# Kernel tuning notes

Hardware: AMD Instinct MI355X
Metric: run time of the kernel (lower is better)

## Reference

```python
import jax, jax.numpy as jnp
import numpy as np
from jax.ops import segment_sum

N_NODES = 100000


def _deg_inv_sqrt(idx, n):
    # DGL GraphConv norm='both': degs clamped to min 1, then deg^{-0.5}
    deg = segment_sum(jnp.ones_like(idx, dtype=jnp.float32), idx, num_segments=n)
    return jnp.where(deg > 0, jax.lax.rsqrt(jnp.maximum(deg, 1.0)), 1.0)


def _graph_conv(x, src, dst, W, b, out_norm, in_norm, n):
    # norm='both': scale src feats by out_deg^-1/2, sum-aggregate, scale by in_deg^-1/2
    h = (x * out_norm[:, None]) @ W          # apply weight first (cheaper/equal width)
    msg = h[src]                              # [E, d] irregular gather
    agg = segment_sum(msg, dst, num_segments=n)
    return agg * in_norm[:, None] + b


def setup_inputs() -> dict:
    key = jax.random.key(0)
    k1, k2, k3, k4, k5, k6, k7 = jax.random.split(key, 7)
    E = 1600000
    in_feats, h_feats, out_feats = 128, 128, 64
    in_feat = jax.random.normal(k1, (N_NODES, in_feats), dtype=jnp.float32)
    src = jax.random.randint(k2, (E,), 0, N_NODES, dtype=jnp.int32)
    dst = jax.random.randint(k3, (E,), 0, N_NODES, dtype=jnp.int32)
    # Glorot-style init like dgl GraphConv
    W1 = jax.random.normal(k4, (in_feats, h_feats), dtype=jnp.float32) * (1.0 / np.sqrt(in_feats))
    b1 = jnp.zeros((h_feats,), dtype=jnp.float32)
    W2 = jax.random.normal(k5, (h_feats, out_feats), dtype=jnp.float32) * (1.0 / np.sqrt(h_feats))
    b2 = jnp.zeros((out_feats,), dtype=jnp.float32)
    return {"in_feat": in_feat, "src": src, "dst": dst, "W1": W1, "b1": b1, "W2": W2, "b2": b2}


def reference(in_feat, src, dst, W1, b1, W2, b2):
    n = in_feat.shape[0]
    out_norm = _deg_inv_sqrt(src, n)  # out-degree norm (source side)
    in_norm = _deg_inv_sqrt(dst, n)   # in-degree norm (destination side)
    h = _graph_conv(in_feat, src, dst, W1, b1, out_norm, in_norm, n)
    z = jax.nn.relu(h)
    h2 = _graph_conv(z, src, dst, W2, b2, out_norm, in_norm, n)
    return (h2, z)
```

## Files before the change

### kernel.cpp

```cpp
#include <hip/hip_runtime.h>

#define N_NODES 100000
#define N_EDGES 1600000
#define NB 391
#define BCAP 5120
#define PART_BLOCKS 250
#define EPB 6400

typedef __attribute__((ext_vector_type(8))) short short8;
typedef __attribute__((ext_vector_type(4))) float f32x4;

__device__ inline unsigned short f2bf(float f) {
    unsigned int u = __builtin_bit_cast(unsigned int, f);
    u += 0x7fffu + ((u >> 16) & 1u);
    return (unsigned short)(u >> 16);
}
__device__ inline float bf2f(unsigned short h) {
    unsigned int u = ((unsigned int)h) << 16;
    return __builtin_bit_cast(float, u);
}

__global__ __launch_bounds__(256) void k_xb(const float* __restrict__ x, const float* __restrict__ out_norm,
                                            unsigned short* __restrict__ xb) {
    int tid = blockIdx.x * 256 + threadIdx.x;
    int row = tid >> 5;
    float4 v = ((const float4*)x)[tid];
    float w = out_norm[row];
    unsigned int lo = (unsigned int)f2bf(v.x * w) | ((unsigned int)f2bf(v.y * w) << 16);
    unsigned int hi = (unsigned int)f2bf(v.z * w) | ((unsigned int)f2bf(v.w * w) << 16);
    ((uint2*)xb)[tid] = make_uint2(lo, hi);
}

__global__ __launch_bounds__(256) void k_pack_w(const float* __restrict__ W1, const float* __restrict__ W2,
                                                unsigned short* __restrict__ Wp1, unsigned short* __restrict__ Wp2) {
    int i = blockIdx.x * 256 + threadIdx.x;
    if (i < 2048) {
        int kq = i >> 7, c = i & 127;
#pragma unroll
        for (int j = 0; j < 8; j++) Wp1[i * 8 + j] = f2bf(W1[(kq * 8 + j) * 128 + c]);
    } else if (i < 3072) {
        int i2 = i - 2048;
        int kq = i2 >> 6, c = i2 & 63;
#pragma unroll
        for (int j = 0; j < 8; j++) Wp2[i2 * 8 + j] = f2bf(W2[(kq * 8 + j) * 64 + c]);
    }
}

__global__ __launch_bounds__(256) void k_part(const int* __restrict__ src, const int* __restrict__ dst,
                                              int* __restrict__ gcurD, int* __restrict__ gcurS,
                                              unsigned int* __restrict__ ebuf,
                                              unsigned char* __restrict__ ebufS) {
    __shared__ int histD[NB], gbaseD[NB];
    __shared__ int histS[NB], gbaseS[NB];
    for (int i = threadIdx.x; i < NB; i += 256) { histD[i] = 0; histS[i] = 0; }
    __syncthreads();
    int base = blockIdx.x * EPB;
    for (int i = threadIdx.x; i < EPB; i += 256) {
        int d = dst[base + i], s = src[base + i];
        atomicAdd(&histD[d >> 8], 1);
        atomicAdd(&histS[s >> 8], 1);
    }
    __syncthreads();
    for (int i = threadIdx.x; i < NB; i += 256) {
        gbaseD[i] = atomicAdd(&gcurD[i], histD[i]);
        gbaseS[i] = atomicAdd(&gcurS[i], histS[i]);
        histD[i] = 0;
        histS[i] = 0;
    }
    __syncthreads();
    for (int i = threadIdx.x; i < EPB; i += 256) {
        int d = dst[base + i], s = src[base + i];
        int bd = d >> 8;
        int r = atomicAdd(&histD[bd], 1);
        int pos = gbaseD[bd] + r;
        if (pos < BCAP) ebuf[(size_t)bd * BCAP + pos] = ((unsigned int)s << 8) | (unsigned int)(d & 255);
        int bs = s >> 8;
        int r2 = atomicAdd(&histS[bs], 1);
        int pos2 = gbaseS[bs] + r2;
        if (pos2 < BCAP) ebufS[(size_t)bs * BCAP + pos2] = (unsigned char)(s & 255);
    }
}

__global__ __launch_bounds__(256) void k_bhist(const unsigned char* __restrict__ ebufS,
                                               const int* __restrict__ gcurS,
                                               float* __restrict__ out_norm) {
    __shared__ int hist[256];
    int b = blockIdx.x, t = threadIdx.x;
    hist[t] = 0;
    __syncthreads();
    int ne = min(gcurS[b], BCAP);
    const unsigned char* eb = ebufS + (size_t)b * BCAP;
    for (int i = t; i < ne; i += 256) atomicAdd(&hist[eb[i]], 1);
    __syncthreads();
    int node = b * 256 + t;
    if (node < N_NODES) out_norm[node] = hist[t] > 0 ? rsqrtf((float)hist[t]) : 1.0f;
}

__global__ __launch_bounds__(512) void k_bscan(const int* __restrict__ gcurD, int* __restrict__ bbase,
                                               int* __restrict__ row_ptr) {
    __shared__ int s[NB + 1];
    int t = threadIdx.x;
    if (t < NB) s[t] = min(gcurD[t], BCAP);
    __syncthreads();
    if (t == 0) {
        int run = 0;
        for (int b = 0; b < NB; b++) { int v = s[b]; s[b] = run; run += v; }
        s[NB] = run;
    }
    __syncthreads();
    if (t < NB) bbase[t] = s[t];
    if (t == 0) { bbase[NB] = s[NB]; row_ptr[N_NODES] = s[NB]; }
}

__global__ __launch_bounds__(256) void k_bsort(const unsigned int* __restrict__ ebuf, const int* __restrict__ gcurD,
                                               const int* __restrict__ bbase, int* __restrict__ csr_src,
                                               int* __restrict__ row_ptr, float* __restrict__ in_norm) {
    __shared__ unsigned int st[BCAP];
    __shared__ int perm[BCAP];
    __shared__ int hist[256], cursor[256], sa[256], sb[256];
    int b = blockIdx.x, t = threadIdx.x;
    int ne = min(gcurD[b], BCAP);
    const unsigned int* eb = ebuf + (size_t)b * BCAP;
    hist[t] = 0;
    __syncthreads();
    for (int i = t; i < ne; i += 256) {
        unsigned int pk = eb[i];
        st[i] = pk;
        atomicAdd(&hist[pk & 255u], 1);
    }
    __syncthreads();
    sa[t] = hist[t];
    __syncthreads();
    int* cur = sa; int* nxt = sb;
    for (int o = 1; o < 256; o <<= 1) {
        int v = cur[t] + (t >= o ? cur[t - o] : 0);
        nxt[t] = v;
        __syncthreads();
        int* tmp = cur; cur = nxt; nxt = tmp;
    }
    int ex = cur[t] - hist[t];
    cursor[t] = ex;
    int node = b * 256 + t;
    if (node < N_NODES) {
        row_ptr[node] = bbase[b] + ex;
        in_norm[node] = hist[t] > 0 ? rsqrtf((float)hist[t]) : 1.0f;
    }
    __syncthreads();
    for (int i = t; i < ne; i += 256) {
        unsigned int pk = st[i];
        int pos = atomicAdd(&cursor[pk & 255u], 1);
        perm[pos] = (int)(pk >> 8);
    }
    __syncthreads();
    int gb = bbase[b];
    for (int i = t; i < ne; i += 256) csr_src[gb + i] = perm[i];
}

__global__ __launch_bounds__(256) void k_agg1(const unsigned short* __restrict__ xb,
                                              const int* __restrict__ row_ptr, const int* __restrict__ csr,
                                              const float* __restrict__ in_norm,
                                              unsigned short* __restrict__ aggb) {
    int wave = threadIdx.x >> 6, lane = threadIdx.x & 63;
    int d = blockIdx.x * 4 + wave;
    if (d >= N_NODES) return;
    int e0 = __builtin_amdgcn_readfirstlane(row_ptr[d]);
    int e1 = __builtin_amdgcn_readfirstlane(row_ptr[d + 1]);
    int col = lane << 1;
    float accL[8], accH[8];
#pragma unroll
    for (int j = 0; j < 8; j++) { accL[j] = 0.f; accH[j] = 0.f; }
    int e = e0;
    for (; e + 8 <= e1; e += 8) {
        int sI[8];
#pragma unroll
        for (int j = 0; j < 8; j++) sI[j] = __builtin_amdgcn_readfirstlane(csr[e + j]);
        unsigned int v[8];
#pragma unroll
        for (int j = 0; j < 8; j++) v[j] = *(const unsigned int*)(xb + (size_t)sI[j] * 128 + col);
#pragma unroll
        for (int j = 0; j < 8; j++) {
            accL[j] += bf2f((unsigned short)(v[j] & 0xffffu));
            accH[j] += bf2f((unsigned short)(v[j] >> 16));
        }
    }
    for (; e < e1; e++) {
        int s = __builtin_amdgcn_readfirstlane(csr[e]);
        unsigned int v = *(const unsigned int*)(xb + (size_t)s * 128 + col);
        accL[0] += bf2f((unsigned short)(v & 0xffffu));
        accH[0] += bf2f((unsigned short)(v >> 16));
    }
    float a0 = 0.f, a1 = 0.f;
#pragma unroll
    for (int j = 0; j < 8; j++) { a0 += accL[j]; a1 += accH[j]; }
    float w = in_norm[d];
    unsigned int pk = (unsigned int)f2bf(a0 * w) | ((unsigned int)f2bf(a1 * w) << 16);
    *(unsigned int*)(aggb + (size_t)d * 128 + col) = pk;
}

__global__ __launch_bounds__(256) void k_gemm1(const unsigned short* __restrict__ Ab,
                                               const unsigned short* __restrict__ Wp,
                                               const float* __restrict__ bias,
                                               const float* __restrict__ out_norm,
                                               float* __restrict__ z_out,
                                               unsigned short* __restrict__ zs) {
    __shared__ __align__(16) unsigned short lds[16 * 128 * 8];
    {
        const uint4* s4 = (const uint4*)Wp; uint4* d4 = (uint4*)lds;
        for (int i = threadIdx.x; i < 2048; i += 256) d4[i] = s4[i];
    }
    __syncthreads();
    int wave = threadIdx.x >> 6, lane = threadIdx.x & 63;
    int base = (blockIdx.x * 4 + wave) * 16;
    if (base >= N_NODES) return;
    int m = lane & 15, q = lane >> 4;
    short8 a[4];
#pragma unroll
    for (int t = 0; t < 4; t++) a[t] = *(const short8*)(Ab + (size_t)(base + m) * 128 + t * 32 + q * 8);
    f32x4 acc[8];
#pragma unroll
    for (int c = 0; c < 8; c++) acc[c] = (f32x4)(0.f);
#pragma unroll
    for (int ct = 0; ct < 8; ct++) {
#pragma unroll
        for (int t = 0; t < 4; t++) {
            short8 b = *(const short8*)(lds + ((t * 4 + q) * 128 + ct * 16 + m) * 8);
            acc[ct] = __builtin_amdgcn_mfma_f32_16x16x32_bf16(a[t], b, acc[ct], 0, 0, 0);
        }
    }
    float onr[4];
#pragma unroll
    for (int i = 0; i < 4; i++) onr[i] = out_norm[base + q * 4 + i];
#pragma unroll
    for (int ct = 0; ct < 8; ct++) {
        int col = ct * 16 + m;
        float bv = bias[col];
#pragma unroll
        for (int i = 0; i < 4; i++) {
            int row = base + q * 4 + i;
            float v = acc[ct][i] + bv;
            v = v > 0.f ? v : 0.f;
            z_out[(size_t)row * 128 + col] = v;
            zs[(size_t)row * 128 + col] = f2bf(v * onr[i]);
        }
    }
}

__global__ __launch_bounds__(256) void k_gemm2(const unsigned short* __restrict__ Ab,
                                               const unsigned short* __restrict__ Wp,
                                               unsigned short* __restrict__ tb) {
    __shared__ __align__(16) unsigned short lds[16 * 64 * 8];
    {
        const uint4* s4 = (const uint4*)Wp; uint4* d4 = (uint4*)lds;
        for (int i = threadIdx.x; i < 1024; i += 256) d4[i] = s4[i];
    }
    __syncthreads();
    int wave = threadIdx.x >> 6, lane = threadIdx.x & 63;
    int base = (blockIdx.x * 4 + wave) * 16;
    if (base >= N_NODES) return;
    int m = lane & 15, q = lane >> 4;
    short8 a[4];
#pragma unroll
    for (int t = 0; t < 4; t++) a[t] = *(const short8*)(Ab + (size_t)(base + m) * 128 + t * 32 + q * 8);
    f32x4 acc[4];
#pragma unroll
    for (int c = 0; c < 4; c++) acc[c] = (f32x4)(0.f);
#pragma unroll
    for (int ct = 0; ct < 4; ct++) {
#pragma unroll
        for (int t = 0; t < 4; t++) {
            short8 b = *(const short8*)(lds + ((t * 4 + q) * 64 + ct * 16 + m) * 8);
            acc[ct] = __builtin_amdgcn_mfma_f32_16x16x32_bf16(a[t], b, acc[ct], 0, 0, 0);
        }
    }
#pragma unroll
    for (int ct = 0; ct < 4; ct++) {
        int col = ct * 16 + m;
#pragma unroll
        for (int i = 0; i < 4; i++) {
            int row = base + q * 4 + i;
            tb[(size_t)row * 64 + col] = f2bf(acc[ct][i]);
        }
    }
}

__global__ __launch_bounds__(256) void k_agg2(const unsigned short* __restrict__ tb,
                                              const int* __restrict__ row_ptr, const int* __restrict__ csr,
                                              const float* __restrict__ in_norm, const float* __restrict__ b2,
                                              float* __restrict__ out_h2) {
    int wave = threadIdx.x >> 6, lane = threadIdx.x & 63;
    int d = blockIdx.x * 4 + wave;
    if (d >= N_NODES) return;
    int e0 = __builtin_amdgcn_readfirstlane(row_ptr[d]);
    int e1 = __builtin_amdgcn_readfirstlane(row_ptr[d + 1]);
    float acc[8];
#pragma unroll
    for (int j = 0; j < 8; j++) acc[j] = 0.f;
    int e = e0;
    for (; e + 8 <= e1; e += 8) {
        int sI[8];
#pragma unroll
        for (int j = 0; j < 8; j++) sI[j] = __builtin_amdgcn_readfirstlane(csr[e + j]);
        unsigned short v[8];
#pragma unroll
        for (int j = 0; j < 8; j++) v[j] = tb[(size_t)sI[j] * 64 + lane];
#pragma unroll
        for (int j = 0; j < 8; j++) acc[j] += bf2f(v[j]);
    }
    for (; e < e1; e++) {
        int s = __builtin_amdgcn_readfirstlane(csr[e]);
        acc[0] += bf2f(tb[(size_t)s * 64 + lane]);
    }
    float a = 0.f;
#pragma unroll
    for (int j = 0; j < 8; j++) a += acc[j];
    out_h2[(size_t)d * 64 + lane] = a * in_norm[d] + b2[lane];
}

extern "C" void kernel_launch(void* const* d_in, const int* in_sizes, int n_in,
                              void* d_out, int out_size, void* d_ws, size_t ws_size,
                              hipStream_t stream) {
    const float* x   = (const float*)d_in[0];
    const int*   src = (const int*)d_in[1];
    const int*   dst = (const int*)d_in[2];
    const float* W1  = (const float*)d_in[3];
    const float* b1  = (const float*)d_in[4];
    const float* W2  = (const float*)d_in[5];
    const float* b2  = (const float*)d_in[6];
    float* out_h2 = (float*)d_out;
    float* out_z  = (float*)d_out + N_NODES * 64;

    char* ws = (char*)d_ws;
    size_t off = 0;
    auto alloc = [&](size_t bytes) -> char* {
        char* p = ws + off;
        off = (off + bytes + 255) & ~(size_t)255;
        return p;
    };
    int* gcurD    = (int*)alloc(NB * 4);
    int* gcurS    = (int*)alloc(NB * 4);
    int* bbase    = (int*)alloc((NB + 1) * 4);
    int* row_ptr  = (int*)alloc((N_NODES + 1) * 4);
    float* out_norm = (float*)alloc(N_NODES * 4);
    float* in_norm  = (float*)alloc(N_NODES * 4);
    unsigned int* ebuf = (unsigned int*)alloc((size_t)NB * BCAP * 4);
    unsigned char* ebufS = (unsigned char*)alloc((size_t)NB * BCAP);
    int* csr_src  = (int*)alloc((size_t)N_EDGES * 4);
    unsigned short* Wp1 = (unsigned short*)alloc(2048 * 8 * 2);
    unsigned short* Wp2 = (unsigned short*)alloc(1024 * 8 * 2);
    unsigned short* xb    = (unsigned short*)alloc((size_t)N_NODES * 128 * 2);
    unsigned short* agg1b = (unsigned short*)alloc((size_t)N_NODES * 128 * 2);
    unsigned short* zs    = (unsigned short*)alloc((size_t)N_NODES * 128 * 2);
    unsigned short* tb    = (unsigned short*)alloc((size_t)N_NODES * 64 * 2);
    (void)ws_size; (void)in_sizes; (void)n_in; (void)out_size;

    hipMemsetAsync(gcurD, 0, NB * 4, stream);
    hipMemsetAsync(gcurS, 0, NB * 4, stream);

    const int GD_AGG = (N_NODES + 3) / 4;
    const int GD_GEMM = (N_NODES / 16 + 3) / 4;

    k_part<<<PART_BLOCKS, 256, 0, stream>>>(src, dst, gcurD, gcurS, ebuf, ebufS);
    k_bhist<<<NB, 256, 0, stream>>>(ebufS, gcurS, out_norm);
    k_bscan<<<1, 512, 0, stream>>>(gcurD, bbase, row_ptr);
    k_bsort<<<NB, 256, 0, stream>>>(ebuf, gcurD, bbase, csr_src, row_ptr, in_norm);
    k_xb<<<N_NODES * 32 / 256, 256, 0, stream>>>(x, out_norm, xb);
    k_pack_w<<<12, 256, 0, stream>>>(W1, W2, Wp1, Wp2);
    k_agg1<<<GD_AGG, 256, 0, stream>>>(xb, row_ptr, csr_src, in_norm, agg1b);
    k_gemm1<<<GD_GEMM, 256, 0, stream>>>(agg1b, Wp1, b1, out_norm, out_z, zs);
    k_gemm2<<<GD_GEMM, 256, 0, stream>>>(zs, Wp2, tb);
    k_agg2<<<GD_AGG, 256, 0, stream>>>(tb, row_ptr, csr_src, in_norm, b2, out_h2);
}
```

Baseline: 337.7 us.

## Fuse both GEMMs into one kernel via LDS and unroll gather loops by 16

The two GEMM kernels are merged: each wave's ReLU'd, out-norm-scaled layer-1 tile is written as bf16 into a padded LDS tile and fed straight into the layer-2 MFMA. This removes the zs global buffer round trip and one kernel launch. Separately, both aggregation kernels gain a 16-edge unrolled loop so more gather loads are in flight per wave. The cost is higher LDS use per block (about 65KB) and more registers, which may reduce occupancy.

```diff
diff --git a/kernel.cpp b/kernel.cpp
--- a/kernel.cpp
+++ b/kernel.cpp
@@ -170,6 +170,19 @@
 #pragma unroll
     for (int j = 0; j < 8; j++) { accL[j] = 0.f; accH[j] = 0.f; }
     int e = e0;
+    for (; e + 16 <= e1; e += 16) {
+        int sI[16];
+#pragma unroll
+        for (int j = 0; j < 16; j++) sI[j] = __builtin_amdgcn_readfirstlane(csr[e + j]);
+        unsigned int v[16];
+#pragma unroll
+        for (int j = 0; j < 16; j++) v[j] = *(const unsigned int*)(xb + (size_t)sI[j] * 128 + col);
+#pragma unroll
+        for (int j = 0; j < 16; j++) {
+            accL[j & 7] += bf2f((unsigned short)(v[j] & 0xffffu));
+            accH[j & 7] += bf2f((unsigned short)(v[j] >> 16));
+        }
+    }
     for (; e + 8 <= e1; e += 8) {
         int sI[8];
 #pragma unroll
@@ -197,16 +210,21 @@
     *(unsigned int*)(aggb + (size_t)d * 128 + col) = pk;
 }
 
-__global__ __launch_bounds__(256) void k_gemm1(const unsigned short* __restrict__ Ab,
-                                               const unsigned short* __restrict__ Wp,
-                                               const float* __restrict__ bias,
-                                               const float* __restrict__ out_norm,
-                                               float* __restrict__ z_out,
-                                               unsigned short* __restrict__ zs) {
-    __shared__ __align__(16) unsigned short lds[16 * 128 * 8];
+__global__ __launch_bounds__(256) void k_gemm12(const unsigned short* __restrict__ Ab,
+                                                const unsigned short* __restrict__ Wp1,
+                                                const unsigned short* __restrict__ Wp2,
+                                                const float* __restrict__ bias1,
+                                                const float* __restrict__ out_norm,
+                                                float* __restrict__ z_out,
+                                                unsigned short* __restrict__ tb) {
+    __shared__ __align__(16) unsigned short lds1[16 * 128 * 8];
+    __shared__ __align__(16) unsigned short lds2[16 * 64 * 8];
+    __shared__ __align__(16) unsigned short zt[64 * 132];
     {
-        const uint4* s4 = (const uint4*)Wp; uint4* d4 = (uint4*)lds;
-        for (int i = threadIdx.x; i < 2048; i += 256) d4[i] = s4[i];
+        const uint4* s1 = (const uint4*)Wp1; uint4* d1 = (uint4*)lds1;
+        for (int i = threadIdx.x; i < 2048; i += 256) d1[i] = s1[i];
+        const uint4* s2 = (const uint4*)Wp2; uint4* d2 = (uint4*)lds2;
+        for (int i = threadIdx.x; i < 1024; i += 256) d2[i] = s2[i];
     }
     __syncthreads();
     int wave = threadIdx.x >> 6, lane = threadIdx.x & 63;
@@ -223,7 +241,7 @@
     for (int ct = 0; ct < 8; ct++) {
 #pragma unroll
         for (int t = 0; t < 4; t++) {
-            short8 b = *(const short8*)(lds + ((t * 4 + q) * 128 + ct * 16 + m) * 8);
+            short8 b = *(const short8*)(lds1 + ((t * 4 + q) * 128 + ct * 16 + m) * 8);
             acc[ct] = __builtin_amdgcn_mfma_f32_16x16x32_bf16(a[t], b, acc[ct], 0, 0, 0);
         }
     }
@@ -233,43 +251,28 @@
 #pragma unroll
     for (int ct = 0; ct < 8; ct++) {
         int col = ct * 16 + m;
-        float bv = bias[col];
+        float bv = bias1[col];
 #pragma unroll
         for (int i = 0; i < 4; i++) {
             int row = base + q * 4 + i;
             float v = acc[ct][i] + bv;
             v = v > 0.f ? v : 0.f;
             z_out[(size_t)row * 128 + col] = v;
-            zs[(size_t)row * 128 + col] = f2bf(v * onr[i]);
-        }
-    }
-}
-
-__global__ __launch_bounds__(256) void k_gemm2(const unsigned short* __restrict__ Ab,
-                                               const unsigned short* __restrict__ Wp,
-                                               unsigned short* __restrict__ tb) {
-    __shared__ __align__(16) unsigned short lds[16 * 64 * 8];
-    {
-        const uint4* s4 = (const uint4*)Wp; uint4* d4 = (uint4*)lds;
-        for (int i = threadIdx.x; i < 1024; i += 256) d4[i] = s4[i];
-    }
-    __syncthreads();
-    int wave = threadIdx.x >> 6, lane = threadIdx.x & 63;
-    int base = (blockIdx.x * 4 + wave) * 16;
-    if (base >= N_NODES) return;
-    int m = lane & 15, q = lane >> 4;
-    short8 a[4];
-#pragma unroll
-    for (int t = 0; t < 4; t++) a[t] = *(const short8*)(Ab + (size_t)(base + m) * 128 + t * 32 + q * 8);
-    f32x4 acc[4];
-#pragma unroll
-    for (int c = 0; c < 4; c++) acc[c] = (f32x4)(0.f);
+            zt[(wave * 16 + q * 4 + i) * 132 + col] = f2bf(v * onr[i]);
+        }
+    }
+    short8 a2[4];
+#pragma unroll
+    for (int t = 0; t < 4; t++) a2[t] = *(const short8*)(zt + (wave * 16 + m) * 132 + t * 32 + q * 8);
+    f32x4 acc2[4];
+#pragma unroll
+    for (int c = 0; c < 4; c++) acc2[c] = (f32x4)(0.f);
 #pragma unroll
     for (int ct = 0; ct < 4; ct++) {
 #pragma unroll
         for (int t = 0; t < 4; t++) {
-            short8 b = *(const short8*)(lds + ((t * 4 + q) * 64 + ct * 16 + m) * 8);
-            acc[ct] = __builtin_amdgcn_mfma_f32_16x16x32_bf16(a[t], b, acc[ct], 0, 0, 0);
+            short8 b = *(const short8*)(lds2 + ((t * 4 + q) * 64 + ct * 16 + m) * 8);
+            acc2[ct] = __builtin_amdgcn_mfma_f32_16x16x32_bf16(a2[t], b, acc2[ct], 0, 0, 0);
         }
     }
 #pragma unroll
@@ -278,7 +281,7 @@
 #pragma unroll
         for (int i = 0; i < 4; i++) {
             int row = base + q * 4 + i;
-            tb[(size_t)row * 64 + col] = f2bf(acc[ct][i]);
+            tb[(size_t)row * 64 + col] = f2bf(acc2[ct][i]);
         }
     }
 }
@@ -296,6 +299,16 @@
 #pragma unroll
     for (int j = 0; j < 8; j++) acc[j] = 0.f;
     int e = e0;
+    for (; e + 16 <= e1; e += 16) {
+        int sI[16];
+#pragma unroll
+        for (int j = 0; j < 16; j++) sI[j] = __builtin_amdgcn_readfirstlane(csr[e + j]);
+        unsigned short v[16];
+#pragma unroll
+        for (int j = 0; j < 16; j++) v[j] = tb[(size_t)sI[j] * 64 + lane];
+#pragma unroll
+        for (int j = 0; j < 16; j++) acc[j & 7] += bf2f(v[j]);
+    }
     for (; e + 8 <= e1; e += 8) {
         int sI[8];
 #pragma unroll
@@ -349,7 +362,6 @@
     unsigned short* Wp2 = (unsigned short*)alloc(1024 * 8 * 2);
     unsigned short* xb    = (unsigned short*)alloc((size_t)N_NODES * 128 * 2);
     unsigned short* agg1b = (unsigned short*)alloc((size_t)N_NODES * 128 * 2);
-    unsigned short* zs    = (unsigned short*)alloc((size_t)N_NODES * 128 * 2);
     unsigned short* tb    = (unsigned short*)alloc((size_t)N_NODES * 64 * 2);
     (void)ws_size; (void)in_sizes; (void)n_in; (void)out_size;
 
@@ -366,7 +378,6 @@
     k_xb<<<N_NODES * 32 / 256, 256, 0, stream>>>(x, out_norm, xb);
     k_pack_w<<<12, 256, 0, stream>>>(W1, W2, Wp1, Wp2);
     k_agg1<<<GD_AGG, 256, 0, stream>>>(xb, row_ptr, csr_src, in_norm, agg1b);
-    k_gemm1<<<GD_GEMM, 256, 0, stream>>>(agg1b, Wp1, b1, out_norm, out_z, zs);
-    k_gemm2<<<GD_GEMM, 256, 0, stream>>>(zs, Wp2, tb);
+    k_gemm12<<<GD_GEMM, 256, 0, stream>>>(agg1b, Wp1, Wp2, b1, out_norm, out_z, tb);
     k_agg2<<<GD_AGG, 256, 0, stream>>>(tb, row_ptr, csr_src, in_norm, b2, out_h2);
 }
```

After: 327.2 us. -3.1%, faster.
